# Optimization experiments

Measured on AMD Instinct MI355X. Metric: run time of the kernel, lower is better.

Reference implementation:

```python
import jax, jax.numpy as jnp
import numpy as np

B, L, E, H = 2, 2048, 1024, 16
HD = E // H


def _rel_shift(x):
    # x: [b, h, q, k] -> Transformer-XL relative shift via pad+reshape trick
    b, h, q, k = x.shape
    xp = jnp.pad(x, ((0, 0), (0, 0), (0, 0), (1, 0)))  # pad left of last dim
    xp = xp.reshape(b, h, k + 1, q)
    return xp[:, :, 1:, :].reshape(b, h, q, k)


def setup_inputs() -> dict:
    key = jax.random.key(0)
    ks = jax.random.split(key, 16)
    s = 0.02
    return {
        "query": jax.random.normal(ks[0], (B, L, E), jnp.float32),
        "key": jax.random.normal(ks[1], (B, L, E), jnp.float32),
        "value": jax.random.normal(ks[2], (B, L, E), jnp.float32),
        "pos_embedding": jax.random.normal(ks[3], (B, L, E), jnp.float32),
        "Wq": jax.random.normal(ks[4], (E, E), jnp.float32) * s,
        "bq": jnp.zeros((E,), jnp.float32),
        "Wk": jax.random.normal(ks[5], (E, E), jnp.float32) * s,
        "bk": jnp.zeros((E,), jnp.float32),
        "Wv": jax.random.normal(ks[6], (E, E), jnp.float32) * s,
        "bv": jnp.zeros((E,), jnp.float32),
        "Wp": jax.random.normal(ks[7], (E, E), jnp.float32) * s,  # Pos linear, no bias
        "Wo": jax.random.normal(ks[8], (E, E), jnp.float32) * s,
        "bo": jnp.zeros((E,), jnp.float32),
        "U": jax.random.normal(ks[9], (H, HD), jnp.float32) * s,
        "V": jax.random.normal(ks[10], (H, HD), jnp.float32) * s,
    }


def reference(query, key, value, pos_embedding, Wq, bq, Wk, bk, Wv, bv, Wp, Wo, bo, U, V):
    b, qlen, e = query.shape
    h, hd = U.shape
    scale = jnp.sqrt(jnp.asarray(e, query.dtype))
    # torch Linear: y = x @ W.T + b
    q = (query @ Wq.T + bq).reshape(b, qlen, h, hd)
    k = (key @ Wk.T + bk).reshape(b, key.shape[1], h, hd)
    v = (value @ Wv.T + bv).reshape(b, value.shape[1], h, hd)
    r = (pos_embedding @ Wp.T).reshape(b, -1, h, hd)
    content_score = jnp.einsum("bqhd,bkhd->bhqk", q + U, k)
    position_score = jnp.einsum("bqhd,bkhd->bhqk", q + V, r)
    position_score = _rel_shift(position_score)
    attention_score = (content_score + position_score) / scale
    # NOTE: the original module applies NO softmax; faithful reproduction.
    # einsum 'bhqk,bvhd->bqhd' sums over both k (scores) and v (values).
    alpha = jnp.einsum("bhqk,bvhd->bqhd", attention_score, v).reshape(b, qlen, e)
    return alpha @ Wo.T + bo
```

## Files before the change

### kernel.cpp

```cpp
#include <hip/hip_runtime.h>

#define BB 2
#define LL 2048
#define EE 1024
#define HH 16
#define HDD 64

typedef __bf16 bf16x8 __attribute__((ext_vector_type(8)));
typedef float f32x4 __attribute__((ext_vector_type(4)));

__device__ __forceinline__ unsigned short f2bf(float f) {
  unsigned int x = __float_as_uint(f);
  return (unsigned short)((x + 0x7FFFu + ((x >> 16) & 1u)) >> 16);
}

__device__ __forceinline__ float bf2f(unsigned short u) {
  return __uint_as_float((unsigned int)u << 16);
}

__device__ __forceinline__ void load_lds16(const void* g, void* l) {
  __builtin_amdgcn_global_load_lds(
      (const __attribute__((address_space(1))) void*)g,
      (__attribute__((address_space(3))) void*)l, 16, 0, 0);
}

#define SUMKV_BLOCKS 256
#define CAST_BLOCKS 1280
#define CAST_STRIDE (CAST_BLOCKS * 256)
__global__ __launch_bounds__(256) void prelude_kernel(
    const float* __restrict__ q, const float* __restrict__ pe,
    const float* __restrict__ wq, const float* __restrict__ wp,
    unsigned short* __restrict__ q16, unsigned short* __restrict__ pe16,
    unsigned short* __restrict__ wq16, unsigned short* __restrict__ wp16,
    const float* __restrict__ key, const float* __restrict__ value,
    float* __restrict__ kpart, float* __restrict__ vpart) {
  if (blockIdx.x < SUMKV_BLOCKS) {
    int blk2 = blockIdx.x;
    int b = blk2 >> 7, ch = blk2 & 127;
    int tid = threadIdx.x;
    const float4* k4 = (const float4*)(key   + ((size_t)b * LL + ch * 16) * EE);
    const float4* v4 = (const float4*)(value + ((size_t)b * LL + ch * 16) * EE);
    float4 ak = make_float4(0.f, 0.f, 0.f, 0.f);
    float4 av = make_float4(0.f, 0.f, 0.f, 0.f);
#pragma unroll 8
    for (int i = 0; i < 16; i++) {
      float4 kk = k4[i * 256 + tid];
      float4 vv = v4[i * 256 + tid];
      ak.x += kk.x; ak.y += kk.y; ak.z += kk.z; ak.w += kk.w;
      av.x += vv.x; av.y += vv.y; av.z += vv.z; av.w += vv.w;
    }
    ((float4*)(kpart + ((size_t)b * 128 + ch) * EE))[tid] = ak;
    ((float4*)(vpart + ((size_t)b * 128 + ch) * EE))[tid] = av;
  } else {
    const int NQ4 = BB * LL * EE / 4;
    const int NW4 = EE * EE / 4;
    int t = (blockIdx.x - SUMKV_BLOCKS) * 256 + threadIdx.x;
    float4 v[8]; unsigned short* dst[8]; int off[8];
#pragma unroll
    for (int k = 0; k < 8; k++) {
      int i = t + k * CAST_STRIDE;
      const float* src;
      if (i < NQ4)                { src = q;  dst[k] = q16;  off[k] = i; }
      else if (i < 2 * NQ4)       { src = pe; dst[k] = pe16; off[k] = i - NQ4; }
      else if (i < 2 * NQ4 + NW4) { src = wq; dst[k] = wq16; off[k] = i - 2 * NQ4; }
      else                        { src = wp; dst[k] = wp16; off[k] = i - 2 * NQ4 - NW4; }
      v[k] = ((const float4*)src)[off[k]];
    }
#pragma unroll
    for (int k = 0; k < 8; k++) {
      ushort4 u;
      u.x = f2bf(v[k].x); u.y = f2bf(v[k].y); u.z = f2bf(v[k].z); u.w = f2bf(v[k].w);
      ((ushort4*)dst[k])[off[k]] = u;
    }
  }
}

__global__ __launch_bounds__(256) void reduce_kernel(
    const float* __restrict__ kpart, const float* __restrict__ vpart,
    float* __restrict__ keysum, float* __restrict__ valsum) {
  int idx = blockIdx.x * 256 + threadIdx.x;
  const float* src = (idx & 2048) ? vpart : kpart;
  float* dst = (idx & 2048) ? valsum : keysum;
  int be = idx & 2047;
  int b = be >> 10, e = be & (EE - 1);
  float s = 0.f;
  for (int c = 0; c < 128; c++) s += src[((size_t)b * 128 + c) * EE + e];
  dst[be] = s;
}

__global__ __launch_bounds__(256) void proj_kernel(
    const float* __restrict__ keysum, const float* __restrict__ valsum,
    const float* __restrict__ Wk, const float* __restrict__ bk,
    const float* __restrict__ Wv, const float* __restrict__ bv,
    float* __restrict__ Kproj, float* __restrict__ Vproj) {
  int wv = threadIdx.x >> 6, lane = threadIdx.x & 63;
  int idx = blockIdx.x * 4 + wv;
  int b = idx >> 10, ep = idx & (EE - 1);
  const float* sum  = blockIdx.z ? valsum : keysum;
  const float* W    = blockIdx.z ? Wv : Wk;
  const float* bias = blockIdx.z ? bv : bk;
  float* outp       = blockIdx.z ? Vproj : Kproj;
  float acc = 0.f;
  for (int k = lane; k < EE; k += 64) acc += sum[b * EE + k] * W[ep * EE + k];
  for (int off = 32; off; off >>= 1) acc += __shfl_down(acc, off, 64);
  if (lane == 0) outp[b * EE + ep] = acc + (float)LL * bias[ep];
}

__global__ __launch_bounds__(256, 3) void gemm_kernel(
    const unsigned short* __restrict__ q16, const unsigned short* __restrict__ wq16,
    const float* __restrict__ bq, unsigned short* __restrict__ qout,
    const unsigned short* __restrict__ pe16, const unsigned short* __restrict__ wp16,
    unsigned short* __restrict__ rout, float* __restrict__ chunks,
    const float* __restrict__ Vproj, const float* __restrict__ Wo,
    float* __restrict__ W2) {
  const int tid = threadIdx.x;
  const int lane = tid & 63;
  const int wv = tid >> 6;

  if (blockIdx.z == 2) {
    int bid = blockIdx.x + 32 * blockIdx.y;
    int wslot = bid * 4 + wv;
    int base = wslot * 32;
    int b = base >> 14;
    int h = (base >> 10) & (HH - 1);
    int e0 = base & (EE - 1);
    float vp = Vproj[b * EE + h * HDD + lane];
    const float* wo = Wo + (size_t)e0 * EE + h * HDD + lane;
    for (int r = 0; r < 32; r++) {
      float acc = vp * wo[(size_t)r * EE];
      for (int off = 32; off; off >>= 1) acc += __shfl_down(acc, off, 64);
      if (lane == 0) W2[((size_t)b * HH + h) * EE + e0 + r] = acc;
    }
    return;
  }

  const int K = EE, N = EE;
  const unsigned short* X; const unsigned short* W; const float* bias;
  unsigned short* Out;
  if (blockIdx.z == 0) { X = q16;  W = wq16; bias = bq;      Out = qout; }
  else                 { X = pe16; W = wp16; bias = nullptr; Out = rout; }

  __shared__ __align__(16) unsigned short As[3][128 * 32];
  __shared__ __align__(16) unsigned short Bs[3][128 * 32];

  const int wr = wv >> 1, wc = wv & 1;
  const int m0 = blockIdx.x * 128;
  const int n0 = blockIdx.y * 128;

  const int srow = wv * 16 + (lane >> 2);
  const int s_src = ((lane & 3) - ((lane >> 3) & 3)) & 3;
  const unsigned short* gA = X + (size_t)(m0 + srow) * K + s_src * 8;
  const unsigned short* gB = W + (size_t)(n0 + srow) * K + s_src * 8;

  f32x4 acc[4][4];
#pragma unroll
  for (int i = 0; i < 4; i++)
#pragma unroll
    for (int j = 0; j < 4; j++) acc[i][j] = (f32x4)0.0f;

  const int arow = wr * 64 + (lane & 15);
  const int brow = wc * 64 + (lane & 15);
  const int koff = (((lane >> 4) + ((lane & 15) >> 1)) & 3) * 8;

#define GSTAGE(BI, KK)                                                    \
  do {                                                                    \
    load_lds16(gA + (KK),                  &As[BI][wv * 512]);            \
    load_lds16(gA + (KK) + (size_t)64 * K, &As[BI][wv * 512 + 2048]);     \
    load_lds16(gB + (KK),                  &Bs[BI][wv * 512]);            \
    load_lds16(gB + (KK) + (size_t)64 * K, &Bs[BI][wv * 512 + 2048]);     \
  } while (0)
#define COMPUTE(BI)                                                       \
  do {                                                                    \
    bf16x8 af[4], bf[4];                                                  \
    _Pragma("unroll") for (int i = 0; i < 4; i++)                         \
      af[i] = *(const bf16x8*)&As[BI][(arow + i * 16) * 32 + koff];       \
    _Pragma("unroll") for (int j = 0; j < 4; j++)                         \
      bf[j] = *(const bf16x8*)&Bs[BI][(brow + j * 16) * 32 + koff];       \
    _Pragma("unroll") for (int i = 0; i < 4; i++)                         \
    _Pragma("unroll") for (int j = 0; j < 4; j++)                         \
      acc[i][j] = __builtin_amdgcn_mfma_f32_16x16x32_bf16(af[i], bf[j],   \
                                                          acc[i][j], 0, 0, 0); \
  } while (0)

  GSTAGE(0, 0);
  GSTAGE(1, 32);
  int c0 = 0, c1 = 1, c2 = 2;
  for (int t = 0; t < 32; ++t) {
    if (t < 31) asm volatile("s_waitcnt vmcnt(4)" ::: "memory");
    else        asm volatile("s_waitcnt vmcnt(0)" ::: "memory");
    __builtin_amdgcn_s_barrier();
    __builtin_amdgcn_sched_barrier(0);
    if (t + 2 < 32) GSTAGE(c2, (t + 2) * 32);
    COMPUTE(c0);
    int tmp = c0; c0 = c1; c1 = c2; c2 = tmp;
  }
#undef GSTAGE
#undef COMPUTE

  const int rbase = m0 + wr * 64 + (lane >> 4) * 4;
  const int cbase = n0 + wc * 64 + (lane & 15);
#pragma unroll
  for (int i = 0; i < 4; i++) {
#pragma unroll
    for (int j = 0; j < 4; j++) {
      int col = cbase + j * 16;
      float badd = bias ? bias[col] : 0.f;
#pragma unroll
      for (int g = 0; g < 4; g++) {
        int row = rbase + i * 16 + g;
        Out[(size_t)row * N + col] = f2bf(acc[i][j][g] + badd);
      }
    }
  }

  if (blockIdx.z == 1) {
    int b = m0 >> 11;
    int ch0 = ((m0 + wr * 64) & (LL - 1)) >> 4;
#pragma unroll
    for (int i = 0; i < 4; i++) {
#pragma unroll
      for (int j = 0; j < 4; j++) {
        float s = acc[i][j][0] + acc[i][j][1] + acc[i][j][2] + acc[i][j][3];
        s += __shfl_down(s, 32, 64);
        s += __shfl_down(s, 16, 64);
        if (lane < 16) {
          int col = n0 + wc * 64 + j * 16 + lane;
          chunks[((size_t)b * 128 + ch0 + i) * EE + col] = s;
        }
      }
    }
  }
}

__global__ __launch_bounds__(256) void scan2f_kernel(
    const unsigned short* __restrict__ qbuf, const unsigned short* __restrict__ rbuf,
    const float* __restrict__ chunks, const float* __restrict__ Kproj,
    const float* __restrict__ U, const float* __restrict__ V,
    float* __restrict__ S1, float* __restrict__ Dbuf) {
  int tid = threadIdx.x, lane = tid & 63;
  int hg = blockIdx.x, ch = blockIdx.y, b = blockIdx.z;
  int e = hg * 256 + tid;
  int h = hg * 4 + (tid >> 6);
  float pre = 0.f, tot = 0.f;
  for (int c = 0; c < 128; c++) {
    float cs = chunks[((size_t)b * 128 + c) * EE + e];
    tot += cs;
    if (c < ch) pre += cs;
  }
  float kp = Kproj[b * EE + e], Ue = U[e], Ve = V[e];
  float run = pre;
  size_t hoff = ((size_t)b * HH + h) * LL;
#pragma unroll 4
  for (int i = 0; i < 16; i++) {
    int m = ch * 16 + i;
    int p = LL - 1 - m;
    float qv = bf2f(qbuf[((size_t)b * LL + p) * EE + e]);
    float rv = bf2f(rbuf[((size_t)b * LL + m) * EE + e]);
    float tq = qv + Ve;
    float d = tq * run;
    float s = tq * tot + (qv + Ue) * kp;
#pragma unroll
    for (int off = 32; off; off >>= 1) {
      d += __shfl_down(d, off, 64);
      s += __shfl_down(s, off, 64);
    }
    if (lane == 0) { Dbuf[hoff + m] = d; S1[hoff + p] = s; }
    run += rv;
  }
}

__global__ __launch_bounds__(256) void out_kernel(
    const float* __restrict__ S1, const float* __restrict__ Dbuf,
    const float* __restrict__ W2, const float* __restrict__ bo,
    float* __restrict__ out) {
  int row0 = blockIdx.x * 8;
  int b = row0 >> 11, p0 = row0 & (LL - 1);
  int tid = threadIdx.x;
  __shared__ float sh[8][HH];
  if (tid < 128) {
    int rr = tid >> 4, h = tid & 15;
    int p = p0 + rr;
    size_t hoff = ((size_t)b * HH + h) * LL;
    float s1 = S1[hoff + p];
    float d1 = Dbuf[hoff + (LL - 1 - p)];
    float d2 = (p == LL - 1) ? 0.f : Dbuf[hoff + (LL - 2 - p)];
    sh[rr][h] = (s1 - d1 + d2) * (1.f / 32.f);
  }
  float4 w2r[HH];
#pragma unroll
  for (int h = 0; h < HH; h++)
    w2r[h] = ((const float4*)(W2 + ((size_t)b * HH + h) * EE))[tid];
  float4 bo4 = ((const float4*)bo)[tid];
  __syncthreads();
#pragma unroll
  for (int rr = 0; rr < 8; rr++) {
    float4 acc = bo4;
#pragma unroll
    for (int h = 0; h < HH; h++) {
      float s = sh[rr][h];
      acc.x += s * w2r[h].x; acc.y += s * w2r[h].y;
      acc.z += s * w2r[h].z; acc.w += s * w2r[h].w;
    }
    ((float4*)out)[(size_t)(row0 + rr) * 256 + tid] = acc;
  }
}

extern "C" void kernel_launch(void* const* d_in, const int* in_sizes, int n_in,
                              void* d_out, int out_size, void* d_ws, size_t ws_size,
                              hipStream_t stream) {
  const float* query = (const float*)d_in[0];
  const float* key   = (const float*)d_in[1];
  const float* value = (const float*)d_in[2];
  const float* pos   = (const float*)d_in[3];
  const float* Wq = (const float*)d_in[4];
  const float* bq = (const float*)d_in[5];
  const float* Wk = (const float*)d_in[6];
  const float* bk = (const float*)d_in[7];
  const float* Wv = (const float*)d_in[8];
  const float* bv = (const float*)d_in[9];
  const float* Wp = (const float*)d_in[10];
  const float* Wo = (const float*)d_in[11];
  const float* bo = (const float*)d_in[12];
  const float* U  = (const float*)d_in[13];
  const float* V  = (const float*)d_in[14];
  float* out = (float*)d_out;

  char* ws = (char*)d_ws;
  size_t o = 0;
  auto take = [&](size_t bytes) -> char* {
    char* p = ws + o;
    o += (bytes + 255) & ~(size_t)255;
    return p;
  };
  float* keysum = (float*)take(BB * EE * 4);
  float* valsum = (float*)take(BB * EE * 4);
  float* Kproj  = (float*)take(BB * EE * 4);
  float* Vproj  = (float*)take(BB * EE * 4);
  float* W2     = (float*)take((size_t)BB * HH * EE * 4);
  float* S1     = (float*)take((size_t)BB * HH * LL * 4);
  float* Dbuf   = (float*)take((size_t)BB * HH * LL * 4);
  float* chunks = (float*)take((size_t)BB * 128 * EE * 4);
  float* kpart  = (float*)take((size_t)BB * 128 * EE * 4);
  float* vpart  = (float*)take((size_t)BB * 128 * EE * 4);
  unsigned short* qbuf = (unsigned short*)take((size_t)BB * LL * EE * 2);
  unsigned short* rbuf = (unsigned short*)take((size_t)BB * LL * EE * 2);
  unsigned short* q16  = (unsigned short*)take((size_t)BB * LL * EE * 2);
  unsigned short* pe16 = (unsigned short*)take((size_t)BB * LL * EE * 2);
  unsigned short* wq16 = (unsigned short*)take((size_t)EE * EE * 2);
  unsigned short* wp16 = (unsigned short*)take((size_t)EE * EE * 2);

  prelude_kernel<<<SUMKV_BLOCKS + CAST_BLOCKS, 256, 0, stream>>>(
      query, pos, Wq, Wp, q16, pe16, wq16, wp16, key, value, kpart, vpart);
  reduce_kernel<<<dim3(16), 256, 0, stream>>>(kpart, vpart, keysum, valsum);
  proj_kernel<<<dim3(BB * EE / 4, 1, 2), 256, 0, stream>>>(
      keysum, valsum, Wk, bk, Wv, bv, Kproj, Vproj);
  gemm_kernel<<<dim3(BB * LL / 128, EE / 128, 3), 256, 0, stream>>>(
      q16, wq16, bq, qbuf, pe16, wp16, rbuf, chunks, Vproj, Wo, W2);
  scan2f_kernel<<<dim3(4, 128, BB), 256, 0, stream>>>(
      qbuf, rbuf, chunks, Kproj, U, V, S1, Dbuf);
  out_kernel<<<dim3(BB * LL / 8), 256, 0, stream>>>(S1, Dbuf, W2, bo, out);
}
```

Measured before the change: 210.4 us.

## Fuse fp32-to-bf16 activation cast into GEMM A-tile loading

Removes the separate cast pass over query and pos_embedding in the prelude kernel. The GEMM now loads fp32 A tiles into registers, converts them to bf16 and writes them to swizzled LDS, while B still uses direct global-to-LDS loads. The pipeline drops from triple to double buffering with __syncthreads, and the occupancy hint goes from 3 to 2. The aim is to avoid writing and re-reading 16 MB of bf16 activations, at the cost of doubled A-load bytes per GEMM block (fp32) and less latency hiding.

```diff
diff --git a/kernel.cpp b/kernel.cpp
--- a/kernel.cpp
+++ b/kernel.cpp
@@ -24,13 +24,17 @@
       (__attribute__((address_space(3))) void*)l, 16, 0, 0);
 }
 
+__device__ __forceinline__ bf16x8 cvt8(float4 lo, float4 hi) {
+  bf16x8 r;
+  r[0] = (__bf16)lo.x; r[1] = (__bf16)lo.y; r[2] = (__bf16)lo.z; r[3] = (__bf16)lo.w;
+  r[4] = (__bf16)hi.x; r[5] = (__bf16)hi.y; r[6] = (__bf16)hi.z; r[7] = (__bf16)hi.w;
+  return r;
+}
+
 #define SUMKV_BLOCKS 256
-#define CAST_BLOCKS 1280
-#define CAST_STRIDE (CAST_BLOCKS * 256)
+#define WCAST_BLOCKS 256
 __global__ __launch_bounds__(256) void prelude_kernel(
-    const float* __restrict__ q, const float* __restrict__ pe,
     const float* __restrict__ wq, const float* __restrict__ wp,
-    unsigned short* __restrict__ q16, unsigned short* __restrict__ pe16,
     unsigned short* __restrict__ wq16, unsigned short* __restrict__ wp16,
     const float* __restrict__ key, const float* __restrict__ value,
     float* __restrict__ kpart, float* __restrict__ vpart) {
@@ -52,25 +56,18 @@
     ((float4*)(kpart + ((size_t)b * 128 + ch) * EE))[tid] = ak;
     ((float4*)(vpart + ((size_t)b * 128 + ch) * EE))[tid] = av;
   } else {
-    const int NQ4 = BB * LL * EE / 4;
     const int NW4 = EE * EE / 4;
     int t = (blockIdx.x - SUMKV_BLOCKS) * 256 + threadIdx.x;
-    float4 v[8]; unsigned short* dst[8]; int off[8];
-#pragma unroll
-    for (int k = 0; k < 8; k++) {
-      int i = t + k * CAST_STRIDE;
-      const float* src;
-      if (i < NQ4)                { src = q;  dst[k] = q16;  off[k] = i; }
-      else if (i < 2 * NQ4)       { src = pe; dst[k] = pe16; off[k] = i - NQ4; }
-      else if (i < 2 * NQ4 + NW4) { src = wq; dst[k] = wq16; off[k] = i - 2 * NQ4; }
-      else                        { src = wp; dst[k] = wp16; off[k] = i - 2 * NQ4 - NW4; }
-      v[k] = ((const float4*)src)[off[k]];
-    }
-#pragma unroll
-    for (int k = 0; k < 8; k++) {
+#pragma unroll
+    for (int k2 = 0; k2 < 8; k2++) {
+      int i = t + k2 * 65536;
+      const float* src = (i < NW4) ? wq : wp;
+      unsigned short* dst = (i < NW4) ? wq16 : wp16;
+      int off = (i < NW4) ? i : i - NW4;
+      float4 v = ((const float4*)src)[off];
       ushort4 u;
-      u.x = f2bf(v[k].x); u.y = f2bf(v[k].y); u.z = f2bf(v[k].z); u.w = f2bf(v[k].w);
-      ((ushort4*)dst[k])[off[k]] = u;
+      u.x = f2bf(v.x); u.y = f2bf(v.y); u.z = f2bf(v.z); u.w = f2bf(v.w);
+      ((ushort4*)dst)[off] = u;
     }
   }
 }
@@ -106,10 +103,10 @@
   if (lane == 0) outp[b * EE + ep] = acc + (float)LL * bias[ep];
 }
 
-__global__ __launch_bounds__(256, 3) void gemm_kernel(
-    const unsigned short* __restrict__ q16, const unsigned short* __restrict__ wq16,
+__global__ __launch_bounds__(256, 2) void gemm_kernel(
+    const float* __restrict__ qf, const unsigned short* __restrict__ wq16,
     const float* __restrict__ bq, unsigned short* __restrict__ qout,
-    const unsigned short* __restrict__ pe16, const unsigned short* __restrict__ wp16,
+    const float* __restrict__ pef, const unsigned short* __restrict__ wp16,
     unsigned short* __restrict__ rout, float* __restrict__ chunks,
     const float* __restrict__ Vproj, const float* __restrict__ Wo,
     float* __restrict__ W2) {
@@ -135,21 +132,24 @@
   }
 
   const int K = EE, N = EE;
-  const unsigned short* X; const unsigned short* W; const float* bias;
+  const float* Xf; const unsigned short* W; const float* bias;
   unsigned short* Out;
-  if (blockIdx.z == 0) { X = q16;  W = wq16; bias = bq;      Out = qout; }
-  else                 { X = pe16; W = wp16; bias = nullptr; Out = rout; }
-
-  __shared__ __align__(16) unsigned short As[3][128 * 32];
-  __shared__ __align__(16) unsigned short Bs[3][128 * 32];
+  if (blockIdx.z == 0) { Xf = qf;  W = wq16; bias = bq;      Out = qout; }
+  else                 { Xf = pef; W = wp16; bias = nullptr; Out = rout; }
+
+  __shared__ __align__(16) unsigned short As[2][128 * 32];
+  __shared__ __align__(16) unsigned short Bs[2][128 * 32];
 
   const int wr = wv >> 1, wc = wv & 1;
   const int m0 = blockIdx.x * 128;
   const int n0 = blockIdx.y * 128;
 
+  const int ar0 = tid >> 2;
+  const int asw = ((tid & 3) + ((tid >> 3) & 3)) & 3;
+  const float* gAf = Xf + (size_t)(m0 + ar0) * K + (tid & 3) * 8;
+
   const int srow = wv * 16 + (lane >> 2);
   const int s_src = ((lane & 3) - ((lane >> 3) & 3)) & 3;
-  const unsigned short* gA = X + (size_t)(m0 + srow) * K + s_src * 8;
   const unsigned short* gB = W + (size_t)(n0 + srow) * K + s_src * 8;
 
   f32x4 acc[4][4];
@@ -162,12 +162,24 @@
   const int brow = wc * 64 + (lane & 15);
   const int koff = (((lane >> 4) + ((lane & 15) >> 1)) & 3) * 8;
 
-#define GSTAGE(BI, KK)                                                    \
+  float4 ra0, ra1, ra2, ra3;
+#define ALOAD(T)                                                          \
   do {                                                                    \
-    load_lds16(gA + (KK),                  &As[BI][wv * 512]);            \
-    load_lds16(gA + (KK) + (size_t)64 * K, &As[BI][wv * 512 + 2048]);     \
-    load_lds16(gB + (KK),                  &Bs[BI][wv * 512]);            \
-    load_lds16(gB + (KK) + (size_t)64 * K, &Bs[BI][wv * 512 + 2048]);     \
+    const float* p = gAf + (T) * 32;                                      \
+    ra0 = *(const float4*)(p);                                            \
+    ra1 = *(const float4*)(p + 4);                                        \
+    ra2 = *(const float4*)(p + (size_t)64 * K);                           \
+    ra3 = *(const float4*)(p + (size_t)64 * K + 4);                       \
+  } while (0)
+#define AWRITE(BI)                                                        \
+  do {                                                                    \
+    *(bf16x8*)&As[BI][ar0 * 32 + asw * 8]        = cvt8(ra0, ra1);        \
+    *(bf16x8*)&As[BI][(64 + ar0) * 32 + asw * 8] = cvt8(ra2, ra3);        \
+  } while (0)
+#define BSTAGE(BI, T)                                                     \
+  do {                                                                    \
+    load_lds16(gB + (T) * 32,                  &Bs[BI][wv * 512]);        \
+    load_lds16(gB + (T) * 32 + (size_t)64 * K, &Bs[BI][wv * 512 + 2048]); \
   } while (0)
 #define COMPUTE(BI)                                                       \
   do {                                                                    \
@@ -182,19 +194,18 @@
                                                           acc[i][j], 0, 0, 0); \
   } while (0)
 
-  GSTAGE(0, 0);
-  GSTAGE(1, 32);
-  int c0 = 0, c1 = 1, c2 = 2;
+  ALOAD(0); BSTAGE(0, 0); AWRITE(0);
+  __syncthreads();
   for (int t = 0; t < 32; ++t) {
-    if (t < 31) asm volatile("s_waitcnt vmcnt(4)" ::: "memory");
-    else        asm volatile("s_waitcnt vmcnt(0)" ::: "memory");
-    __builtin_amdgcn_s_barrier();
-    __builtin_amdgcn_sched_barrier(0);
-    if (t + 2 < 32) GSTAGE(c2, (t + 2) * 32);
-    COMPUTE(c0);
-    int tmp = c0; c0 = c1; c1 = c2; c2 = tmp;
-  }
-#undef GSTAGE
+    int cur = t & 1, nxt = cur ^ 1;
+    if (t + 1 < 32) { ALOAD(t + 1); BSTAGE(nxt, t + 1); }
+    COMPUTE(cur);
+    if (t + 1 < 32) AWRITE(nxt);
+    __syncthreads();
+  }
+#undef ALOAD
+#undef AWRITE
+#undef BSTAGE
 #undef COMPUTE
 
   const int rbase = m0 + wr * 64 + (lane >> 4) * 4;
@@ -344,18 +355,16 @@
   float* vpart  = (float*)take((size_t)BB * 128 * EE * 4);
   unsigned short* qbuf = (unsigned short*)take((size_t)BB * LL * EE * 2);
   unsigned short* rbuf = (unsigned short*)take((size_t)BB * LL * EE * 2);
-  unsigned short* q16  = (unsigned short*)take((size_t)BB * LL * EE * 2);
-  unsigned short* pe16 = (unsigned short*)take((size_t)BB * LL * EE * 2);
   unsigned short* wq16 = (unsigned short*)take((size_t)EE * EE * 2);
   unsigned short* wp16 = (unsigned short*)take((size_t)EE * EE * 2);
 
-  prelude_kernel<<<SUMKV_BLOCKS + CAST_BLOCKS, 256, 0, stream>>>(
-      query, pos, Wq, Wp, q16, pe16, wq16, wp16, key, value, kpart, vpart);
+  prelude_kernel<<<SUMKV_BLOCKS + WCAST_BLOCKS, 256, 0, stream>>>(
+      Wq, Wp, wq16, wp16, key, value, kpart, vpart);
   reduce_kernel<<<dim3(16), 256, 0, stream>>>(kpart, vpart, keysum, valsum);
   proj_kernel<<<dim3(BB * EE / 4, 1, 2), 256, 0, stream>>>(
       keysum, valsum, Wk, bk, Wv, bv, Kproj, Vproj);
   gemm_kernel<<<dim3(BB * LL / 128, EE / 128, 3), 256, 0, stream>>>(
-      q16, wq16, bq, qbuf, pe16, wp16, rbuf, chunks, Vproj, Wo, W2);
+      query, wq16, bq, qbuf, pos, wp16, rbuf, chunks, Vproj, Wo, W2);
   scan2f_kernel<<<dim3(4, 128, BB), 256, 0, stream>>>(
       qbuf, rbuf, chunks, Kproj, U, V, S1, Dbuf);
   out_kernel<<<dim3(BB * LL / 8), 256, 0, stream>>>(S1, Dbuf, W2, bo, out);
```

Result: slower. 218.3 us (+3.8%).
